# Performance work log

Measured on AMD Instinct MI355X. Metric: run time of the kernel, lower is better.

Reference implementation:

```python
import jax, jax.numpy as jnp
import numpy as np

L = 500_000      # total nodes across all graphs
D = 256          # d_model
G = 4096         # number of graphs
EPS_SOFTMAX = 1e-7
EPS_LN = 1e-5


def setup_inputs() -> dict:
    key = jax.random.key(0)
    ks = jax.random.split(key, 6)
    f_node = jax.random.normal(ks[0], (L, D), dtype=jnp.float32)
    key_W = jax.random.normal(ks[1], (D, D), dtype=jnp.float32) * 0.02
    key_b = jnp.zeros((D,), dtype=jnp.float32)
    value_W = jax.random.normal(ks[2], (D, D), dtype=jnp.float32) * 0.02
    value_b = jnp.zeros((D,), dtype=jnp.float32)
    gamma = jnp.ones((D,), dtype=jnp.float32)
    beta = jnp.zeros((D,), dtype=jnp.float32)
    graph_id = jax.random.randint(ks[3], (L,), 0, G, dtype=jnp.int32)
    return {
        "f_node": f_node,
        "key_W": key_W,
        "key_b": key_b,
        "value_W": value_W,
        "value_b": value_b,
        "gamma": gamma,
        "beta": beta,
        "graph_id": graph_id,
        "num_graphs": G,
    }


def reference(f_node, key_W, key_b, value_W, value_b, gamma, beta, graph_id, num_graphs):
    # attn scores: Linear(key)  -> [L, D]
    attn = f_node @ key_W.T + key_b
    # scatter_softmax over nodes within each graph (per feature column)
    seg_max = jax.ops.segment_max(attn, graph_id, num_segments=num_graphs)  # [G, D]
    ex = jnp.exp(attn - seg_max[graph_id])                                   # [L, D]
    seg_sum = jax.ops.segment_sum(ex, graph_id, num_segments=num_graphs)    # [G, D]
    attn = ex / (seg_sum[graph_id] + EPS_SOFTMAX)
    # weighted aggregation of value projection -> [G, D]
    val = f_node @ value_W.T + value_b
    f_graph = jax.ops.segment_sum(val * attn, graph_id, num_segments=num_graphs)
    # LayerNorm (dropout is identity in eval mode)
    mu = jnp.mean(f_graph, axis=-1, keepdims=True)
    var = jnp.mean(jnp.square(f_graph - mu), axis=-1, keepdims=True)
    return (f_graph - mu) * jax.lax.rsqrt(var + EPS_LN) * gamma + beta
```

## Files before the change

### kernel.cpp

```cpp
#include <hip/hip_runtime.h>

typedef short short8 __attribute__((ext_vector_type(8)));
typedef float floatx4 __attribute__((ext_vector_type(4)));

#define ORD_CAP 1024

__device__ __forceinline__ unsigned short f2bf(float x) {
  union { float f; unsigned int u; } c; c.f = x;
  return (unsigned short)((c.u + 0x7FFFu + ((c.u >> 16) & 1u)) >> 16);
}

__device__ __forceinline__ unsigned cvtpk(float lo, float hi) {
  unsigned r;
  asm("v_cvt_pk_bf16_f32 %0, %1, %2" : "=v"(r) : "v"(lo), "v"(hi));
  return r;
}

__device__ __forceinline__ void gld16(const void* g, void* l) {
  __builtin_amdgcn_global_load_lds((const __attribute__((address_space(1))) void*)g,
                                   (__attribute__((address_space(3))) void*)l, 16, 0, 0);
}

__global__ void k_hist(const int* __restrict__ gid, int L, int* __restrict__ counts) {
  int i = blockIdx.x * blockDim.x + threadIdx.x;
  if (i < L) atomicAdd(&counts[gid[i]], 1);
}

__global__ void k_scan(const int* __restrict__ counts, int* __restrict__ offsets,
                       int* __restrict__ cursor, int G) {
  __shared__ int sc[1024];
  int t = threadIdx.x;
  int items = (G + 1023) >> 10;
  int base = t * items;
  int s = 0;
  for (int i = 0; i < items; ++i) { int idx = base + i; if (idx < G) s += counts[idx]; }
  sc[t] = s;
  __syncthreads();
  for (int off = 1; off < 1024; off <<= 1) {
    int v = (t >= off) ? sc[t - off] : 0;
    __syncthreads();
    if (t >= off) sc[t] += v;
    __syncthreads();
  }
  int run = (t == 0) ? 0 : sc[t - 1];
  for (int i = 0; i < items; ++i) {
    int idx = base + i;
    if (idx < G) { offsets[idx] = run; cursor[idx] = run; run += counts[idx]; }
  }
  if (t == 1023) offsets[G] = sc[1023];
}

__global__ void k_scatter(const int* __restrict__ gid, int L, int* __restrict__ cursor,
                          int* __restrict__ order) {
  int i = blockIdx.x * blockDim.x + threadIdx.x;
  if (i < L) {
    int g = gid[i];
    int pos = atomicAdd(&cursor[g], 1);
    order[pos] = i;
  }
}

__global__ void k_prepw(const float* __restrict__ keyW, const float* __restrict__ valW,
                        unsigned short* __restrict__ W2) {
  int j2 = blockIdx.x;
  int k = threadIdx.x;
  int wv = j2 >> 6, half = (j2 >> 5) & 1, c = j2 & 31;
  int d = (wv << 5) + c;
  const float* src = half ? valW : keyW;
  W2[j2 * 256 + k] = f2bf(src[d * 256 + k]);
}

__launch_bounds__(512, 2)
__global__ void k_fused(const float* __restrict__ fnode,
                        const unsigned short* __restrict__ W2,
                        const float* __restrict__ key_b, const float* __restrict__ value_b,
                        const float* __restrict__ gamma, const float* __restrict__ beta,
                        const int* __restrict__ order, const int* __restrict__ offsets,
                        float* __restrict__ out) {
  __shared__ __align__(16) float As[2][64 * 256];
  __shared__ int ord_s[ORD_CAP];
  __shared__ float fg[256];
  __shared__ float red[8];

  const int g = blockIdx.x;
  const int t = threadIdx.x;
  const int lane = t & 63;
  const int w = t >> 6;
  const int lcol = lane & 15;
  const int lrow = lane >> 4;

  const int s0 = offsets[g];
  const int n_g = offsets[g + 1] - s0;
  const int nchunks = (n_g + 63) >> 6;

  float kb[2], vb[2];
#pragma unroll
  for (int nj = 0; nj < 2; ++nj) {
    int d = (w << 5) + (nj << 4) + lcol;
    kb[nj] = key_b[d];
    vb[nj] = value_b[d];
  }

  const unsigned short* Wn[4];
#pragma unroll
  for (int nj = 0; nj < 4; ++nj)
    Wn[nj] = W2 + ((size_t)((w << 6) + ((nj >> 1) << 5) + ((nj & 1) << 4) + lcol)) * 256 +
             lrow * 8;

  short8 bp[4][4];
#pragma unroll
  for (int nj = 0; nj < 4; ++nj)
#pragma unroll
    for (int kk = 0; kk < 4; ++kk)
      bp[nj][kk] = *reinterpret_cast<const short8*>(Wn[nj] + kk * 32);

  for (int i = t; i < ORD_CAP; i += 512) ord_s[i] = (i < n_g) ? order[s0 + i] : 0;
  __syncthreads();

  float den[2] = {0.f, 0.f};
  float num[2] = {0.f, 0.f};

  auto stage = [&](int c, int bsel) {
    const int m0 = c << 6;
    int idx = 0;
    if (lane < 8) {
      int gi = m0 + (w << 3) + lane;
      idx = ord_s[(gi < n_g) ? gi : 0];
    }
#pragma unroll
    for (int it = 0; it < 8; ++it) {
      const int rid = __shfl(idx, it, 64);
      const int rowl = (w << 3) + it;
      const char* gsrc = (const char*)fnode + ((size_t)rid << 10) +
                         ((lane << 4) ^ (it << 4));
      char* ldst = (char*)&As[bsel][0] + (rowl << 10);
      gld16(gsrc, ldst);
    }
  };

  if (nchunks > 0) stage(0, 0);

  for (int c = 0; c < nchunks; ++c) {
    if (c + 1 < nchunks) {
      stage(c + 1, (c + 1) & 1);
      asm volatile("s_waitcnt vmcnt(8)" ::: "memory");
    } else {
      asm volatile("s_waitcnt vmcnt(0)" ::: "memory");
    }
    __builtin_amdgcn_s_barrier();

    const char* AsB = (const char*)&As[c & 1][0];
    floatx4 acc[4][4];
#pragma unroll
    for (int mi = 0; mi < 4; ++mi)
#pragma unroll
      for (int nj = 0; nj < 4; ++nj)
        acc[mi][nj] = (floatx4){0.f, 0.f, 0.f, 0.f};

#pragma unroll
    for (int kk = 0; kk < 8; ++kk) {
      const int kb2 = kk * 128 + lrow * 32;
      short8 afr[4];
#pragma unroll
      for (int mi = 0; mi < 4; ++mi) {
        const int row = mi * 16 + lcol;
        const int sw = (row & 7) << 4;
        const floatx4 lo =
            *reinterpret_cast<const floatx4*>(AsB + (row << 10) + (kb2 ^ sw));
        const floatx4 hi =
            *reinterpret_cast<const floatx4*>(AsB + (row << 10) + ((kb2 + 16) ^ sw));
        union { unsigned u[4]; short8 s; } cc;
        cc.u[0] = cvtpk(lo[0], lo[1]);
        cc.u[1] = cvtpk(lo[2], lo[3]);
        cc.u[2] = cvtpk(hi[0], hi[1]);
        cc.u[3] = cvtpk(hi[2], hi[3]);
        afr[mi] = cc.s;
      }
#pragma unroll
      for (int nj = 0; nj < 4; ++nj) {
        short8 bfr;
        if (kk < 4) bfr = bp[nj][kk];
        else bfr = *reinterpret_cast<const short8*>(Wn[nj] + kk * 32);
#pragma unroll
        for (int mi = 0; mi < 4; ++mi)
          acc[mi][nj] =
              __builtin_amdgcn_mfma_f32_16x16x32_bf16(afr[mi], bfr, acc[mi][nj], 0, 0, 0);
      }
    }

    const int valid = min(64, n_g - (c << 6));
#pragma unroll
    for (int mi = 0; mi < 4; ++mi) {
#pragma unroll
      for (int qq = 0; qq < 4; ++qq) {
        const int r = mi * 16 + lrow * 4 + qq;
        const bool mvalid = (r < valid);
#pragma unroll
        for (int nj = 0; nj < 2; ++nj) {
          const float a = acc[mi][nj][qq] + kb[nj];
          const float v = acc[mi][nj + 2][qq] + vb[nj];
          const float e = mvalid ? __expf(a) : 0.f;
          den[nj] += e;
          num[nj] += v * e;
        }
      }
    }

    asm volatile("" ::: "memory");
    __builtin_amdgcn_s_barrier();
  }

#pragma unroll
  for (int nj = 0; nj < 2; ++nj) {
    float ds = den[nj], ns = num[nj];
    ds += __shfl_xor(ds, 16, 64);
    ds += __shfl_xor(ds, 32, 64);
    ns += __shfl_xor(ns, 16, 64);
    ns += __shfl_xor(ns, 32, 64);
    if (lrow == 0) fg[(w << 5) + (nj << 4) + lcol] = ns / (ds + 1e-7f);
  }
  __syncthreads();

  float x = 0.f;
  if (t < 256) x = fg[t];
  float s = x, s2 = x * x;
#pragma unroll
  for (int o = 32; o > 0; o >>= 1) {
    s += __shfl_xor(s, o, 64);
    s2 += __shfl_xor(s2, o, 64);
  }
  if (t < 256 && lane == 0) { red[w] = s; red[4 + w] = s2; }
  __syncthreads();
  if (t < 256) {
    const float ts = red[0] + red[1] + red[2] + red[3];
    const float ts2 = red[4] + red[5] + red[6] + red[7];
    const float mu = ts * (1.f / 256.f);
    const float var = ts2 * (1.f / 256.f) - mu * mu;
    const float inv = rsqrtf(var + 1e-5f);
    out[(size_t)g * 256 + t] = (x - mu) * inv * gamma[t] + beta[t];
  }
}

extern "C" void kernel_launch(void* const* d_in, const int* in_sizes, int n_in,
                              void* d_out, int out_size, void* d_ws, size_t ws_size,
                              hipStream_t stream) {
  const float* f_node   = (const float*)d_in[0];
  const float* key_W    = (const float*)d_in[1];
  const float* key_b    = (const float*)d_in[2];
  const float* value_W  = (const float*)d_in[3];
  const float* value_b  = (const float*)d_in[4];
  const float* gamma    = (const float*)d_in[5];
  const float* beta     = (const float*)d_in[6];
  const int*   graph_id = (const int*)d_in[7];
  const int L = in_sizes[0] / 256;
  const int G = out_size / 256;

  char* ws = (char*)d_ws;
  size_t off = 0;
  int* order = (int*)(ws + off); off += (size_t)L * 4;
  off = (off + 255) & ~(size_t)255;
  int* counts = (int*)(ws + off); off += (size_t)G * 4;
  int* offsets = (int*)(ws + off); off += (size_t)(G + 1) * 4;
  int* cursor = (int*)(ws + off); off += (size_t)G * 4;
  off = (off + 255) & ~(size_t)255;
  unsigned short* W2 = (unsigned short*)(ws + off); off += 512 * 256 * 2;

  hipMemsetAsync(counts, 0, (size_t)G * 4, stream);
  k_hist<<<(L + 255) / 256, 256, 0, stream>>>(graph_id, L, counts);
  k_scan<<<1, 1024, 0, stream>>>(counts, offsets, cursor, G);
  k_scatter<<<(L + 255) / 256, 256, 0, stream>>>(graph_id, L, cursor, order);
  k_prepw<<<512, 256, 0, stream>>>(key_W, value_W, W2);
  k_fused<<<G, 512, 0, stream>>>(f_node, W2, key_b, value_b, gamma, beta, order, offsets,
                                 (float*)d_out);
}
```

Before: 450.2 us.

## Pack multiple graphs per block and pre-convert staged rows to bf16 in LDS

Each block now handles 8 consecutive graphs and processes their sorted nodes as one continuous stream of 64-row chunks. This removes the padding waste from partial chunks, since each graph averages about 122 nodes. Graph boundaries are handled inside a chunk by masked segment accumulation, and each finished graph is flushed through LayerNorm. Staged fp32 rows are converted once into a double-buffered, swizzled bf16 LDS tile instead of being converted per MFMA fragment load, and order indices are prefetched asynchronously. The cost is extra barriers per chunk, a fully waited single fp32 staging buffer that gives less overlap, and fewer blocks (512), which may reduce occupancy across CUs.

```diff
diff --git a/kernel.cpp b/kernel.cpp
--- a/kernel.cpp
+++ b/kernel.cpp
@@ -3,7 +3,7 @@
 typedef short short8 __attribute__((ext_vector_type(8)));
 typedef float floatx4 __attribute__((ext_vector_type(4)));
 
-#define ORD_CAP 1024
+#define GPB 8
 
 __device__ __forceinline__ unsigned short f2bf(float x) {
   union { float f; unsigned int u; } c; c.f = x;
@@ -19,6 +19,10 @@
 __device__ __forceinline__ void gld16(const void* g, void* l) {
   __builtin_amdgcn_global_load_lds((const __attribute__((address_space(1))) void*)g,
                                    (__attribute__((address_space(3))) void*)l, 16, 0, 0);
+}
+__device__ __forceinline__ void gld4(const void* g, void* l) {
+  __builtin_amdgcn_global_load_lds((const __attribute__((address_space(1))) void*)g,
+                                   (__attribute__((address_space(3))) void*)l, 4, 0, 0);
 }
 
 __global__ void k_hist(const int* __restrict__ gid, int L, int* __restrict__ counts) {
@@ -76,22 +80,26 @@
                         const float* __restrict__ key_b, const float* __restrict__ value_b,
                         const float* __restrict__ gamma, const float* __restrict__ beta,
                         const int* __restrict__ order, const int* __restrict__ offsets,
-                        float* __restrict__ out) {
-  __shared__ __align__(16) float As[2][64 * 256];
-  __shared__ int ord_s[ORD_CAP];
-  __shared__ float fg[256];
-  __shared__ float red[8];
-
-  const int g = blockIdx.x;
+                        float* __restrict__ out, int L, int Gtot) {
+  __shared__ __align__(16) float f32stage[64 * 256];
+  __shared__ __align__(16) unsigned short bfA[2][64 * 256];
+  __shared__ float fg[GPB][256];
+  __shared__ int ord_ring[2][64];
+  __shared__ int eb[GPB + 1];
+  __shared__ float redS[4], redS2[4];
+
   const int t = threadIdx.x;
   const int lane = t & 63;
   const int w = t >> 6;
   const int lcol = lane & 15;
   const int lrow = lane >> 4;
-
-  const int s0 = offsets[g];
-  const int n_g = offsets[g + 1] - s0;
-  const int nchunks = (n_g + 63) >> 6;
+  const int g0 = blockIdx.x * GPB;
+
+  if (t <= GPB) eb[t] = offsets[min(g0 + t, Gtot)];
+  __syncthreads();
+  const int rbase = eb[0];
+  const int nrows = eb[GPB] - rbase;
+  const int nc = max(1, (nrows + 63) >> 6);
 
   float kb[2], vb[2];
 #pragma unroll
@@ -114,42 +122,67 @@
     for (int kk = 0; kk < 4; ++kk)
       bp[nj][kk] = *reinterpret_cast<const short8*>(Wn[nj] + kk * 32);
 
-  for (int i = t; i < ORD_CAP; i += 512) ord_s[i] = (i < n_g) ? order[s0 + i] : 0;
-  __syncthreads();
-
   float den[2] = {0.f, 0.f};
   float num[2] = {0.f, 0.f};
 
-  auto stage = [&](int c, int bsel) {
+  auto stage_ord = [&](int c) {
+    if (w == 0) {
+      int pos = rbase + (c << 6) + lane;
+      if (pos >= L) pos = L - 1;
+      gld4(order + pos, &ord_ring[c & 1][0]);
+    }
+  };
+  auto stage_rows = [&](int c) {
+#pragma unroll
+    for (int it = 0; it < 8; ++it) {
+      const int idx = ord_ring[c & 1][(w << 3) + it];
+      const char* gsrc =
+          (const char*)fnode + ((size_t)idx << 10) + ((lane << 4) ^ (it << 4));
+      gld16(gsrc, (char*)f32stage + (((w << 3) + it) << 10));
+    }
+  };
+
+  int curg = 0;
+  int ecur = eb[1] - rbase;
+  int flushed = 0;
+
+  stage_ord(0);
+  asm volatile("s_waitcnt vmcnt(0)" ::: "memory");
+  __syncthreads();
+  stage_rows(0);
+  if (nc > 1) stage_ord(1);
+
+  for (int c = 0; c < nc; ++c) {
     const int m0 = c << 6;
-    int idx = 0;
-    if (lane < 8) {
-      int gi = m0 + (w << 3) + lane;
-      idx = ord_s[(gi < n_g) ? gi : 0];
-    }
-#pragma unroll
-    for (int it = 0; it < 8; ++it) {
-      const int rid = __shfl(idx, it, 64);
-      const int rowl = (w << 3) + it;
-      const char* gsrc = (const char*)fnode + ((size_t)rid << 10) +
-                         ((lane << 4) ^ (it << 4));
-      char* ldst = (char*)&As[bsel][0] + (rowl << 10);
-      gld16(gsrc, ldst);
-    }
-  };
-
-  if (nchunks > 0) stage(0, 0);
-
-  for (int c = 0; c < nchunks; ++c) {
-    if (c + 1 < nchunks) {
-      stage(c + 1, (c + 1) & 1);
-      asm volatile("s_waitcnt vmcnt(8)" ::: "memory");
-    } else {
-      asm volatile("s_waitcnt vmcnt(0)" ::: "memory");
-    }
-    __builtin_amdgcn_s_barrier();
-
-    const char* AsB = (const char*)&As[c & 1][0];
+
+    asm volatile("s_waitcnt vmcnt(0)" ::: "memory");
+    __syncthreads();
+
+    {
+      const int r = t >> 3, q = t & 7, x7 = r & 7;
+      const char* fsrow = (const char*)f32stage + (r << 10);
+      char* bfrow = (char*)&bfA[c & 1][0] + (r << 9);
+#pragma unroll
+      for (int i = 0; i < 4; ++i) {
+        const int S0 = 8 * q + 2 * i;
+        const floatx4 a = *(const floatx4*)(fsrow + ((S0 ^ x7) << 4));
+        const floatx4 b2 = *(const floatx4*)(fsrow + (((S0 + 1) ^ x7) << 4));
+        uint4 o;
+        o.x = cvtpk(a[0], a[1]);
+        o.y = cvtpk(a[2], a[3]);
+        o.z = cvtpk(b2[0], b2[1]);
+        o.w = cvtpk(b2[2], b2[3]);
+        *(uint4*)(bfrow + (((4 * q + i) ^ x7) << 4)) = o;
+      }
+    }
+    __syncthreads();
+
+    if (c + 1 < nc) {
+      stage_rows(c + 1);
+      if (c + 2 < nc) stage_ord(c + 2);
+    }
+
+    const char* bfb = (const char*)&bfA[c & 1][0];
     floatx4 acc[4][4];
 #pragma unroll
     for (int mi = 0; mi < 4; ++mi)
@@ -157,87 +190,95 @@
       for (int nj = 0; nj < 4; ++nj)
         acc[mi][nj] = (floatx4){0.f, 0.f, 0.f, 0.f};
 
+    __builtin_amdgcn_s_setprio(1);
 #pragma unroll
     for (int kk = 0; kk < 8; ++kk) {
-      const int kb2 = kk * 128 + lrow * 32;
       short8 afr[4];
 #pragma unroll
       for (int mi = 0; mi < 4; ++mi) {
         const int row = mi * 16 + lcol;
-        const int sw = (row & 7) << 4;
-        const floatx4 lo =
-            *reinterpret_cast<const floatx4*>(AsB + (row << 10) + (kb2 ^ sw));
-        const floatx4 hi =
-            *reinterpret_cast<const floatx4*>(AsB + (row << 10) + ((kb2 + 16) ^ sw));
-        union { unsigned u[4]; short8 s; } cc;
-        cc.u[0] = cvtpk(lo[0], lo[1]);
-        cc.u[1] = cvtpk(lo[2], lo[3]);
-        cc.u[2] = cvtpk(hi[0], hi[1]);
-        cc.u[3] = cvtpk(hi[2], hi[3]);
-        afr[mi] = cc.s;
+        afr[mi] = *reinterpret_cast<const short8*>(
+            bfb + (row << 9) + ((((kk << 2) + lrow) ^ (row & 7)) << 4));
       }
 #pragma unroll
       for (int nj = 0; nj < 4; ++nj) {
-        short8 bfr;
-        if (kk < 4) bfr = bp[nj][kk];
-        else bfr = *reinterpret_cast<const short8*>(Wn[nj] + kk * 32);
+        const short8 bfr = (kk < 4)
+                               ? bp[nj][kk]
+                               : *reinterpret_cast<const short8*>(Wn[nj] + (kk << 5));
 #pragma unroll
         for (int mi = 0; mi < 4; ++mi)
           acc[mi][nj] =
               __builtin_amdgcn_mfma_f32_16x16x32_bf16(afr[mi], bfr, acc[mi][nj], 0, 0, 0);
       }
     }
-
-    const int valid = min(64, n_g - (c << 6));
-#pragma unroll
-    for (int mi = 0; mi < 4; ++mi) {
-#pragma unroll
-      for (int qq = 0; qq < 4; ++qq) {
-        const int r = mi * 16 + lrow * 4 + qq;
-        const bool mvalid = (r < valid);
-#pragma unroll
-        for (int nj = 0; nj < 2; ++nj) {
-          const float a = acc[mi][nj][qq] + kb[nj];
-          const float v = acc[mi][nj + 2][qq] + vb[nj];
-          const float e = mvalid ? __expf(a) : 0.f;
-          den[nj] += e;
-          num[nj] += v * e;
+    __builtin_amdgcn_s_setprio(0);
+
+    {
+      int lo = 0;
+      while (true) {
+        const int hi = min(ecur - m0, 64);
+#pragma unroll
+        for (int mi = 0; mi < 4; ++mi)
+#pragma unroll
+          for (int qq = 0; qq < 4; ++qq) {
+            const int r = mi * 16 + lrow * 4 + qq;
+            const bool in = (r >= lo) && (r < hi);
+#pragma unroll
+            for (int nj = 0; nj < 2; ++nj) {
+              const float a = acc[mi][nj][qq] + kb[nj];
+              const float v = acc[mi][nj + 2][qq] + vb[nj];
+              const float e_ = in ? __expf(a) : 0.f;
+              den[nj] += e_;
+              num[nj] += v * e_;
+            }
+          }
+        if (ecur <= m0 + 64) {
+#pragma unroll
+          for (int nj = 0; nj < 2; ++nj) {
+            float ds = den[nj], ns = num[nj];
+            ds += __shfl_xor(ds, 16, 64);
+            ds += __shfl_xor(ds, 32, 64);
+            ns += __shfl_xor(ns, 16, 64);
+            ns += __shfl_xor(ns, 32, 64);
+            if (lrow == 0)
+              fg[curg & (GPB - 1)][(w << 5) + (nj << 4) + lcol] = ns / (ds + 1e-7f);
+            den[nj] = 0.f;
+            num[nj] = 0.f;
+          }
+          ++curg;
+          lo = hi;
+          ecur = (curg < GPB) ? (eb[curg + 1] - rbase) : 0x7fffffff;
+        } else
+          break;
+        if (curg >= GPB) break;
+      }
+    }
+
+    if (curg > flushed) {
+      __syncthreads();
+      for (int j = flushed; j < curg; ++j) {
+        float x = 0.f;
+        if (t < 256) x = fg[j & (GPB - 1)][t];
+        float s = x, s2 = x * x;
+#pragma unroll
+        for (int o = 32; o > 0; o >>= 1) {
+          s += __shfl_xor(s, o, 64);
+          s2 += __shfl_xor(s2, o, 64);
         }
-      }
-    }
-
-    asm volatile("" ::: "memory");
-    __builtin_amdgcn_s_barrier();
-  }
-
-#pragma unroll
-  for (int nj = 0; nj < 2; ++nj) {
-    float ds = den[nj], ns = num[nj];
-    ds += __shfl_xor(ds, 16, 64);
-    ds += __shfl_xor(ds, 32, 64);
-    ns += __shfl_xor(ns, 16, 64);
-    ns += __shfl_xor(ns, 32, 64);
-    if (lrow == 0) fg[(w << 5) + (nj << 4) + lcol] = ns / (ds + 1e-7f);
-  }
-  __syncthreads();
-
-  float x = 0.f;
-  if (t < 256) x = fg[t];
-  float s = x, s2 = x * x;
-#pragma unroll
-  for (int o = 32; o > 0; o >>= 1) {
-    s += __shfl_xor(s, o, 64);
-    s2 += __shfl_xor(s2, o, 64);
-  }
-  if (t < 256 && lane == 0) { red[w] = s; red[4 + w] = s2; }
-  __syncthreads();
-  if (t < 256) {
-    const float ts = red[0] + red[1] + red[2] + red[3];
-    const float ts2 = red[4] + red[5] + red[6] + red[7];
-    const float mu = ts * (1.f / 256.f);
-    const float var = ts2 * (1.f / 256.f) - mu * mu;
-    const float inv = rsqrtf(var + 1e-5f);
-    out[(size_t)g * 256 + t] = (x - mu) * inv * gamma[t] + beta[t];
+        if (t < 256 && lane == 0) { redS[w] = s; redS2[w] = s2; }
+        __syncthreads();
+        if (t < 256 && (g0 + j) < Gtot) {
+          const float ts = redS[0] + redS[1] + redS[2] + redS[3];
+          const float ts2 = redS2[0] + redS2[1] + redS2[2] + redS2[3];
+          const float mu = ts * (1.f / 256.f);
+          const float var = ts2 * (1.f / 256.f) - mu * mu;
+          const float inv = rsqrtf(var + 1e-5f);
+          out[(size_t)(g0 + j) * 256 + t] = (x - mu) * inv * gamma[t] + beta[t];
+        }
+        __syncthreads();
+      }
+      flushed = curg;
+    }
   }
 }
 
@@ -270,6 +311,7 @@
   k_scan<<<1, 1024, 0, stream>>>(counts, offsets, cursor, G);
   k_scatter<<<(L + 255) / 256, 256, 0, stream>>>(graph_id, L, cursor, order);
   k_prepw<<<512, 256, 0, stream>>>(key_W, value_W, W2);
-  k_fused<<<G, 512, 0, stream>>>(f_node, W2, key_b, value_b, gamma, beta, order, offsets,
-                                 (float*)d_out);
-}
+  const int nblk = (G + GPB - 1) / GPB;
+  k_fused<<<nblk, 512, 0, stream>>>(f_node, W2, key_b, value_b, gamma, beta, order,
+                                    offsets, (float*)d_out, L, G);
+}
```

After: 376.2 us. 1.2x faster.
